# Optimization experiments

Hardware: AMD Instinct MI355X
Metric: run time of the kernel (lower is better)

Reference implementation:

```python
import jax, jax.numpy as jnp
import numpy as np

S, B, H = 2048, 2, 1024
NH = 16
HD = H // NH  # 64


def setup_inputs() -> dict:
    key = jax.random.key(0)
    k1, k2 = jax.random.split(key)
    hidden_states = jax.random.normal(k1, (S, B, H), dtype=jnp.float32)
    W_qkv = jax.random.normal(k2, (3 * H, H), dtype=jnp.float32) * (H ** -0.5)
    b_qkv = jnp.zeros((3 * H,), dtype=jnp.float32)
    return {"hidden_states": hidden_states, "W_qkv": W_qkv, "b_qkv": b_qkv}


def reference(hidden_states, W_qkv, b_qkv):
    s, b, h = hidden_states.shape
    # QKV projection: [S,B,3H] -> [S,B,NH,3*HD] -> split
    qkv = hidden_states @ W_qkv.T + b_qkv
    qkv = qkv.reshape(s, b, NH, 3 * HD)
    q, k, v = jnp.split(qkv, 3, axis=-1)  # each [S,B,NH,HD]
    norm_factor = HD ** -0.5
    # scores: [B,NH,Sq,Sk]
    scores = jnp.einsum('sbhd,tbhd->bhst', q, k) * norm_factor
    # Cumsum sequence-op (seq_op_in_fp32=True): cumsum over key dim, scaled by Sq^-0.5
    probs = jnp.cumsum(scores.astype(jnp.float32), axis=-1) * (s ** -0.5)
    probs = probs.astype(hidden_states.dtype)
    # PV: [B,NH,Sq,HD] -> seq-first [Sq,B,NH*HD]
    ctx = jnp.einsum('bhst,tbhd->sbhd', probs, v)
    return ctx.reshape(s, b, h)
```

## Files before the change

### kernel.cpp

```cpp
#include <hip/hip_runtime.h>

#define S 2048
#define B 2
#define H 1024
#define NH 16
#define HD 64
#define THREE_H 3072
#define ROWS (S*B)

typedef __attribute__((ext_vector_type(8))) short short8;
typedef __attribute__((ext_vector_type(4))) float f32x4;
typedef const __attribute__((address_space(1))) unsigned int* gptr_t;
typedef __attribute__((address_space(3))) unsigned int* lptr_t;

#define N8_A (ROWS * H / 8)
#define N8_W (THREE_H * H / 8)

__device__ __forceinline__ ushort f2bf(float f) {
    union { float f; unsigned u; } v; v.f = f;
    unsigned r = v.u + 0x7fffu + ((v.u >> 16) & 1u);
    return (ushort)(r >> 16);
}

__global__ void cast_both(const float* __restrict__ A, const float* __restrict__ W,
                          ushort* __restrict__ Ab, ushort* __restrict__ Wb) {
    int i = blockIdx.x * 256 + threadIdx.x;
    const float4* s4;
    ushort* dst;
    if (i < N8_A) { s4 = (const float4*)A; dst = Ab; }
    else if (i < N8_A + N8_W) { s4 = (const float4*)W; dst = Wb; i -= N8_A; }
    else return;
    float4 a = s4[2 * i], b = s4[2 * i + 1];
    short8 o;
    o[0] = f2bf(a.x); o[1] = f2bf(a.y); o[2] = f2bf(a.z); o[3] = f2bf(a.w);
    o[4] = f2bf(b.x); o[5] = f2bf(b.y); o[6] = f2bf(b.z); o[7] = f2bf(b.w);
    *(short8*)(dst + 8 * (size_t)i) = o;
}

__global__ __launch_bounds__(256) void qkv_gemm_mfma(const ushort* __restrict__ Abf,
                                                     const ushort* __restrict__ Wbf,
                                                     const float* __restrict__ bias,
                                                     ushort* __restrict__ Qb,
                                                     ushort* __restrict__ Kb,
                                                     float* __restrict__ Vf) {
    __shared__ ushort Abuf[128 * 32];
    __shared__ ushort Bbuf[128 * 32];
    const int tid = threadIdx.x;
    const int wave = tid >> 6, lane = tid & 63;
    const int wr = wave >> 1, wc = wave & 1;
    const int row0 = blockIdx.x * 128;
    const int col0 = blockIdx.y * 128;

    f32x4 acc[4][4] = {};

    const int lrow = lane >> 2;
    const int lk   = (lane & 3) * 8;

    for (int k0 = 0; k0 < H; k0 += 32) {
#pragma unroll
        for (int p = 0; p < 2; ++p) {
            int c = wave * 2 + p;
            int row = c * 16 + lrow;
            __builtin_amdgcn_global_load_lds(
                (gptr_t)&Abf[(size_t)(row0 + row) * H + k0 + lk],
                (lptr_t)&Abuf[c * 512 + lane * 8], 16, 0, 0);
            __builtin_amdgcn_global_load_lds(
                (gptr_t)&Wbf[(size_t)(col0 + row) * H + k0 + lk],
                (lptr_t)&Bbuf[c * 512 + lane * 8], 16, 0, 0);
        }
        __syncthreads();

        short8 af[4], bfr[4];
#pragma unroll
        for (int m = 0; m < 4; ++m) {
            int ar = wr * 64 + m * 16 + (lane & 15);
            af[m] = *(const short8*)&Abuf[ar * 32 + (lane >> 4) * 8];
            int br = wc * 64 + m * 16 + (lane & 15);
            bfr[m] = *(const short8*)&Bbuf[br * 32 + (lane >> 4) * 8];
        }
#pragma unroll
        for (int m = 0; m < 4; ++m)
#pragma unroll
            for (int n = 0; n < 4; ++n)
                acc[m][n] = __builtin_amdgcn_mfma_f32_16x16x32_bf16(af[m], bfr[n], acc[m][n], 0, 0, 0);
        __syncthreads();
    }

#pragma unroll
    for (int n = 0; n < 4; ++n) {
        int cbase = col0 + wc * 64 + n * 16;
        int h   = cbase / 192;
        int r3  = cbase % 192;
        int sel = r3 >> 6;
        int d   = (r3 & 63) + (lane & 15);
        float bv = bias[cbase + (lane & 15)];
#pragma unroll
        for (int m = 0; m < 4; ++m) {
            int rowb = row0 + wr * 64 + m * 16 + (lane >> 4) * 4;
#pragma unroll
            for (int j = 0; j < 4; ++j) {
                int r = rowb + j;
                int s = r >> 1, b = r & 1;
                size_t off = ((size_t)((b * NH + h) * S + s)) * HD + d;
                float val = acc[m][n][j] + bv;
                if (sel == 0)      Qb[off] = f2bf(val);
                else if (sel == 1) Kb[off] = f2bf(val);
                else               Vf[off] = val;
            }
        }
    }
}

__global__ void vsuf_chunksum(const float* __restrict__ Vf, float* __restrict__ csum) {
    int idx = blockIdx.x * 256 + threadIdx.x;
    int col = idx & 2047;
    int chunk = idx >> 11;
    const float* vp = Vf + ((size_t)(col >> 6) * S + chunk * 32) * HD + (col & 63);
    float s = 0.f;
#pragma unroll
    for (int t = 0; t < 32; ++t) s += vp[(size_t)t * HD];
    csum[idx] = s;
}

__global__ void vsuft_final(const float* __restrict__ Vf, const float* __restrict__ csum,
                            ushort* __restrict__ Vt) {
    int idx = blockIdx.x * 256 + threadIdx.x;
    int col = idx & 2047;
    int chunk = idx >> 11;
    int bh = col >> 6, d = col & 63;
    float acc = 0.f;
    for (int c = chunk + 1; c < 64; ++c) acc += csum[c * 2048 + col];
    const float* vp = Vf + ((size_t)bh * S + chunk * 32) * HD + d;
    ushort buf[32];
#pragma unroll
    for (int tt = 31; tt >= 0; --tt) {
        acc += vp[(size_t)tt * HD];
        buf[tt] = f2bf(acc);
    }
    ushort* op = Vt + ((size_t)bh * HD + d) * S + chunk * 32;
#pragma unroll
    for (int q = 0; q < 4; ++q) {
        short8 o;
#pragma unroll
        for (int k = 0; k < 8; ++k) o[k] = buf[q * 8 + k];
        *(short8*)(op + q * 8) = o;
    }
}

__global__ __launch_bounds__(256) void ktrans(const ushort* __restrict__ Kb,
                                              ushort* __restrict__ Kt) {
    __shared__ ushort Ks[64][72];
    const int bh = blockIdx.x;
    const int t0 = blockIdx.y * 64;
    const int tid = threadIdx.x;
    {
        const int tt = tid >> 2, part = (tid & 3) * 16;
        const ushort* src = Kb + ((size_t)bh * S + t0 + tt) * HD + part;
        *(short8*)&Ks[tt][part]     = *(const short8*)(src);
        *(short8*)&Ks[tt][part + 8] = *(const short8*)(src + 8);
    }
    __syncthreads();
    {
        const int d = tid >> 2, tq = (tid & 3) * 16;
        ushort tmp[16];
#pragma unroll
        for (int k = 0; k < 16; ++k) tmp[k] = Ks[tq + k][d];
        ushort* dst = Kt + ((size_t)bh * HD + d) * S + t0 + tq;
        short8 o0, o1;
#pragma unroll
        for (int k = 0; k < 8; ++k) { o0[k] = tmp[k]; o1[k] = tmp[8 + k]; }
        *(short8*)dst = o0;
        *(short8*)(dst + 8) = o1;
    }
}

__global__ __launch_bounds__(256) void kvm_mfma(const ushort* __restrict__ Kt,
                                                const ushort* __restrict__ Vt,
                                                float* __restrict__ Mpart) {
    const int bh = blockIdx.x, kb = blockIdx.y;
    const int tid = threadIdx.x, wave = tid >> 6, lane = tid & 63;
    const int slice = kb * 4 + wave;
    const ushort* Kp = Kt + (size_t)bh * HD * S;
    const ushort* Vp = Vt + (size_t)bh * HD * S;
    f32x4 acc[4][4] = {};
    const int il = lane & 15;
    const int tbase = slice * 128 + (lane >> 4) * 8;
#pragma unroll
    for (int ks = 0; ks < 4; ++ks) {
        const int t = tbase + ks * 32;
        short8 af[4], bfv[4];
#pragma unroll
        for (int m = 0; m < 4; ++m) af[m]  = *(const short8*)&Kp[(size_t)(m * 16 + il) * S + t];
#pragma unroll
        for (int n = 0; n < 4; ++n) bfv[n] = *(const short8*)&Vp[(size_t)(n * 16 + il) * S + t];
#pragma unroll
        for (int m = 0; m < 4; ++m)
#pragma unroll
            for (int n = 0; n < 4; ++n)
                acc[m][n] = __builtin_amdgcn_mfma_f32_16x16x32_bf16(af[m], bfv[n], acc[m][n], 0, 0, 0);
    }
    float* Mp = Mpart + ((size_t)slice * 32 + bh) * 4096;
#pragma unroll
    for (int m = 0; m < 4; ++m)
#pragma unroll
        for (int n = 0; n < 4; ++n)
#pragma unroll
            for (int j = 0; j < 4; ++j) {
                int i  = m * 16 + (lane >> 4) * 4 + j;
                int jj = n * 16 + il;
                Mp[i * 64 + jj] = acc[m][n][j];
            }
}

__global__ __launch_bounds__(256) void qm_mfma(const ushort* __restrict__ Qb,
                                               const float* __restrict__ Mpart,
                                               float* __restrict__ out) {
    __shared__ ushort Mt[64][72];
    const int bh = blockIdx.x, b = bh >> 4, h = bh & 15;
    const int tid = threadIdx.x;
    {
        const int i = tid >> 2, jq = (tid & 3) * 16;
        f32x4 s0 = {}, s1 = {}, s2 = {}, s3 = {};
#pragma unroll
        for (int sl = 0; sl < 16; ++sl) {
            const float* p = Mpart + ((size_t)sl * 32 + bh) * 4096 + i * 64 + jq;
            s0 += *(const f32x4*)(p);
            s1 += *(const f32x4*)(p + 4);
            s2 += *(const f32x4*)(p + 8);
            s3 += *(const f32x4*)(p + 12);
        }
#pragma unroll
        for (int k = 0; k < 4; ++k) {
            Mt[jq + 0  + k][i] = f2bf(s0[k]);
            Mt[jq + 4  + k][i] = f2bf(s1[k]);
            Mt[jq + 8  + k][i] = f2bf(s2[k]);
            Mt[jq + 12 + k][i] = f2bf(s3[k]);
        }
    }
    __syncthreads();
    const int wave = tid >> 6, lane = tid & 63;
    const int sl15 = lane & 15, koct = (lane >> 4) * 8;
    const int s0b = blockIdx.y * 256 + wave * 64;
    f32x4 acc[4][4] = {};
#pragma unroll
    for (int ks = 0; ks < 2; ++ks) {
        short8 af[4], bfv[4];
#pragma unroll
        for (int m = 0; m < 4; ++m) {
            int s = s0b + m * 16 + sl15;
            af[m] = *(const short8*)&Qb[((size_t)bh * S + s) * HD + ks * 32 + koct];
        }
#pragma unroll
        for (int n = 0; n < 4; ++n)
            bfv[n] = *(const short8*)&Mt[n * 16 + sl15][ks * 32 + koct];
#pragma unroll
        for (int m = 0; m < 4; ++m)
#pragma unroll
            for (int n = 0; n < 4; ++n)
                acc[m][n] = __builtin_amdgcn_mfma_f32_16x16x32_bf16(af[m], bfv[n], acc[m][n], 0, 0, 0);
    }
    const float scale = 0.125f * 0.02209708691207961f;
#pragma unroll
    for (int m = 0; m < 4; ++m)
#pragma unroll
        for (int n = 0; n < 4; ++n)
#pragma unroll
            for (int j = 0; j < 4; ++j) {
                int s = s0b + m * 16 + (lane >> 4) * 4 + j;
                int d = n * 16 + sl15;
                out[(size_t)(s * B + b) * H + h * 64 + d] = acc[m][n][j] * scale;
            }
}

extern "C" void kernel_launch(void* const* d_in, const int* in_sizes, int n_in,
                              void* d_out, int out_size, void* d_ws, size_t ws_size,
                              hipStream_t stream) {
    const float* hidden = (const float*)d_in[0];
    const float* W      = (const float*)d_in[1];
    const float* bias   = (const float*)d_in[2];
    float* out = (float*)d_out;

    float*  Vf    = (float*)d_ws;
    ushort* Qb    = (ushort*)(Vf + 4194304);
    ushort* Kb    = Qb + 4194304;
    ushort* Kt    = Kb + 4194304;
    ushort* Vt    = Kt + 4194304;
    float*  csum  = (float*)(Vt + 4194304);
    float*  Mpart = csum + 131072;
    ushort* Abf   = (ushort*)(Mpart + 2097152);
    ushort* Wbf   = Abf + 4194304;

    cast_both<<<(N8_A + N8_W + 255) / 256, 256, 0, stream>>>(hidden, W, Abf, Wbf);
    qkv_gemm_mfma<<<dim3(ROWS / 128, THREE_H / 128), 256, 0, stream>>>(Abf, Wbf, bias, Qb, Kb, Vf);
    vsuf_chunksum<<<512, 256, 0, stream>>>(Vf, csum);
    vsuft_final<<<512, 256, 0, stream>>>(Vf, csum, Vt);
    ktrans<<<dim3(32, 32), 256, 0, stream>>>(Kb, Kt);
    kvm_mfma<<<dim3(32, 4), 256, 0, stream>>>(Kt, Vt, Mpart);
    qm_mfma<<<dim3(32, 8), 256, 0, stream>>>(Qb, Mpart, out);
}
```

Baseline: 86.16 us.

## Widen GEMM K-tile with XOR-swizzled LDS, store V as bf16, merge ktrans with chunksum

The QKV GEMM now loads 64-wide K tiles per barrier, with an XOR swizzle on LDS slots to avoid bank conflicts, and remaps workgroups so neighbouring blocks share tiles in L2. V is written as bf16 instead of fp32, which halves its write and read traffic. The K transpose and the V chunk-sum kernels are fused into one launch, removing a launch and letting both run concurrently. Storing V in bf16 before the suffix sum adds a small precision loss in the prefix accumulation.

```diff
diff --git a/kernel.cpp b/kernel.cpp
--- a/kernel.cpp
+++ b/kernel.cpp
@@ -20,6 +20,10 @@
     union { float f; unsigned u; } v; v.f = f;
     unsigned r = v.u + 0x7fffu + ((v.u >> 16) & 1u);
     return (ushort)(r >> 16);
+}
+__device__ __forceinline__ float bf2f(ushort u) {
+    union { unsigned u; float f; } v; v.u = ((unsigned)u) << 16;
+    return v.f;
 }
 
 __global__ void cast_both(const float* __restrict__ A, const float* __restrict__ W,
@@ -42,47 +46,58 @@
                                                      const float* __restrict__ bias,
                                                      ushort* __restrict__ Qb,
                                                      ushort* __restrict__ Kb,
-                                                     float* __restrict__ Vf) {
-    __shared__ ushort Abuf[128 * 32];
-    __shared__ ushort Bbuf[128 * 32];
+                                                     ushort* __restrict__ Vraw) {
+    __shared__ ushort Abuf[128 * 64];
+    __shared__ ushort Bbuf[128 * 64];
     const int tid = threadIdx.x;
     const int wave = tid >> 6, lane = tid & 63;
     const int wr = wave >> 1, wc = wave & 1;
-    const int row0 = blockIdx.x * 128;
-    const int col0 = blockIdx.y * 128;
+
+    const int wgid = blockIdx.y * 32 + blockIdx.x;
+    const int swz = (wgid & 7) * 96 + (wgid >> 3);
+    const int row0 = (swz & 31) * 128;
+    const int col0 = (swz >> 5) * 128;
 
     f32x4 acc[4][4] = {};
 
-    const int lrow = lane >> 2;
-    const int lk   = (lane & 3) * 8;
-
-    for (int k0 = 0; k0 < H; k0 += 32) {
-#pragma unroll
-        for (int p = 0; p < 2; ++p) {
-            int c = wave * 2 + p;
-            int row = c * 16 + lrow;
+    const int srow = lane >> 3;
+    const int gk = ((lane & 7) ^ srow) * 8;
+    const int il = lane & 15, ko = lane >> 4;
+
+    for (int k0 = 0; k0 < H; k0 += 64) {
+#pragma unroll
+        for (int p = 0; p < 4; ++p) {
+            int row = wave * 32 + p * 8 + srow;
             __builtin_amdgcn_global_load_lds(
-                (gptr_t)&Abf[(size_t)(row0 + row) * H + k0 + lk],
-                (lptr_t)&Abuf[c * 512 + lane * 8], 16, 0, 0);
+                (gptr_t)&Abf[(size_t)(row0 + row) * H + k0 + gk],
+                (lptr_t)&Abuf[(wave * 32 + p * 8) * 64 + lane * 8], 16, 0, 0);
             __builtin_amdgcn_global_load_lds(
-                (gptr_t)&Wbf[(size_t)(col0 + row) * H + k0 + lk],
-                (lptr_t)&Bbuf[c * 512 + lane * 8], 16, 0, 0);
+                (gptr_t)&Wbf[(size_t)(col0 + row) * H + k0 + gk],
+                (lptr_t)&Bbuf[(wave * 32 + p * 8) * 64 + lane * 8], 16, 0, 0);
         }
         __syncthreads();
 
-        short8 af[4], bfr[4];
+        short8 af[4][2], bfr[4][2];
 #pragma unroll
         for (int m = 0; m < 4; ++m) {
-            int ar = wr * 64 + m * 16 + (lane & 15);
-            af[m] = *(const short8*)&Abuf[ar * 32 + (lane >> 4) * 8];
-            int br = wc * 64 + m * 16 + (lane & 15);
-            bfr[m] = *(const short8*)&Bbuf[br * 32 + (lane >> 4) * 8];
-        }
-#pragma unroll
-        for (int m = 0; m < 4; ++m)
-#pragma unroll
-            for (int n = 0; n < 4; ++n)
-                acc[m][n] = __builtin_amdgcn_mfma_f32_16x16x32_bf16(af[m], bfr[n], acc[m][n], 0, 0, 0);
+            int ar = wr * 64 + m * 16 + il;
+            int br = wc * 64 + m * 16 + il;
+#pragma unroll
+            for (int ks = 0; ks < 2; ++ks) {
+                int aslot = (ks * 4 + ko) ^ (ar & 7);
+                int bslot = (ks * 4 + ko) ^ (br & 7);
+                af[m][ks]  = *(const short8*)&Abuf[ar * 64 + aslot * 8];
+                bfr[m][ks] = *(const short8*)&Bbuf[br * 64 + bslot * 8];
+            }
+        }
+#pragma unroll
+        for (int ks = 0; ks < 2; ++ks)
+#pragma unroll
+            for (int m = 0; m < 4; ++m)
+#pragma unroll
+                for (int n = 0; n < 4; ++n)
+                    acc[m][n] = __builtin_amdgcn_mfma_f32_16x16x32_bf16(
+                        af[m][ks], bfr[n][ks], acc[m][n], 0, 0, 0);
         __syncthreads();
     }
 
@@ -92,37 +107,64 @@
         int h   = cbase / 192;
         int r3  = cbase % 192;
         int sel = r3 >> 6;
-        int d   = (r3 & 63) + (lane & 15);
-        float bv = bias[cbase + (lane & 15)];
+        int d   = (r3 & 63) + il;
+        float bv = bias[cbase + il];
+        ushort* dst = (sel == 0) ? Qb : (sel == 1) ? Kb : Vraw;
 #pragma unroll
         for (int m = 0; m < 4; ++m) {
-            int rowb = row0 + wr * 64 + m * 16 + (lane >> 4) * 4;
+            int rowb = row0 + wr * 64 + m * 16 + ko * 4;
 #pragma unroll
             for (int j = 0; j < 4; ++j) {
                 int r = rowb + j;
                 int s = r >> 1, b = r & 1;
-                size_t off = ((size_t)((b * NH + h) * S + s)) * HD + d;
-                float val = acc[m][n][j] + bv;
-                if (sel == 0)      Qb[off] = f2bf(val);
-                else if (sel == 1) Kb[off] = f2bf(val);
-                else               Vf[off] = val;
+                dst[((size_t)((b * NH + h) * S + s)) * HD + d] = f2bf(acc[m][n][j] + bv);
             }
         }
     }
 }
 
-__global__ void vsuf_chunksum(const float* __restrict__ Vf, float* __restrict__ csum) {
-    int idx = blockIdx.x * 256 + threadIdx.x;
-    int col = idx & 2047;
-    int chunk = idx >> 11;
-    const float* vp = Vf + ((size_t)(col >> 6) * S + chunk * 32) * HD + (col & 63);
-    float s = 0.f;
-#pragma unroll
-    for (int t = 0; t < 32; ++t) s += vp[(size_t)t * HD];
-    csum[idx] = s;
-}
-
-__global__ void vsuft_final(const float* __restrict__ Vf, const float* __restrict__ csum,
+__global__ __launch_bounds__(256) void ktrans_chunksum(const ushort* __restrict__ Kb,
+                                                       ushort* __restrict__ Kt,
+                                                       const ushort* __restrict__ Vraw,
+                                                       float* __restrict__ csum) {
+    __shared__ ushort Ks[64][72];
+    const int gb = blockIdx.x;
+    const int tid = threadIdx.x;
+    if (gb < 1024) {
+        const int bh = gb >> 5;
+        const int t0 = (gb & 31) * 64;
+        {
+            const int tt = tid >> 2, part = (tid & 3) * 16;
+            const ushort* src = Kb + ((size_t)bh * S + t0 + tt) * HD + part;
+            *(short8*)&Ks[tt][part]     = *(const short8*)(src);
+            *(short8*)&Ks[tt][part + 8] = *(const short8*)(src + 8);
+        }
+        __syncthreads();
+        {
+            const int d = tid >> 2, tq = (tid & 3) * 16;
+            ushort tmp[16];
+#pragma unroll
+            for (int k = 0; k < 16; ++k) tmp[k] = Ks[tq + k][d];
+            ushort* dst = Kt + ((size_t)bh * HD + d) * S + t0 + tq;
+            short8 o0, o1;
+#pragma unroll
+            for (int k = 0; k < 8; ++k) { o0[k] = tmp[k]; o1[k] = tmp[8 + k]; }
+            *(short8*)dst = o0;
+            *(short8*)(dst + 8) = o1;
+        }
+    } else {
+        int idx = (gb - 1024) * 256 + tid;
+        int col = idx & 2047;
+        int chunk = idx >> 11;
+        const ushort* vp = Vraw + ((size_t)(col >> 6) * S + chunk * 32) * HD + (col & 63);
+        float s = 0.f;
+#pragma unroll
+        for (int t = 0; t < 32; ++t) s += bf2f(vp[(size_t)t * HD]);
+        csum[chunk * 2048 + col] = s;
+    }
+}
+
+__global__ void vsuft_final(const ushort* __restrict__ Vraw, const float* __restrict__ csum,
                             ushort* __restrict__ Vt) {
     int idx = blockIdx.x * 256 + threadIdx.x;
     int col = idx & 2047;
@@ -130,11 +172,11 @@
     int bh = col >> 6, d = col & 63;
     float acc = 0.f;
     for (int c = chunk + 1; c < 64; ++c) acc += csum[c * 2048 + col];
-    const float* vp = Vf + ((size_t)bh * S + chunk * 32) * HD + d;
+    const ushort* vp = Vraw + ((size_t)bh * S + chunk * 32) * HD + d;
     ushort buf[32];
 #pragma unroll
     for (int tt = 31; tt >= 0; --tt) {
-        acc += vp[(size_t)tt * HD];
+        acc += bf2f(vp[(size_t)tt * HD]);
         buf[tt] = f2bf(acc);
     }
     ushort* op = Vt + ((size_t)bh * HD + d) * S + chunk * 32;
@@ -144,33 +186,6 @@
 #pragma unroll
         for (int k = 0; k < 8; ++k) o[k] = buf[q * 8 + k];
         *(short8*)(op + q * 8) = o;
-    }
-}
-
-__global__ __launch_bounds__(256) void ktrans(const ushort* __restrict__ Kb,
-                                              ushort* __restrict__ Kt) {
-    __shared__ ushort Ks[64][72];
-    const int bh = blockIdx.x;
-    const int t0 = blockIdx.y * 64;
-    const int tid = threadIdx.x;
-    {
-        const int tt = tid >> 2, part = (tid & 3) * 16;
-        const ushort* src = Kb + ((size_t)bh * S + t0 + tt) * HD + part;
-        *(short8*)&Ks[tt][part]     = *(const short8*)(src);
-        *(short8*)&Ks[tt][part + 8] = *(const short8*)(src + 8);
-    }
-    __syncthreads();
-    {
-        const int d = tid >> 2, tq = (tid & 3) * 16;
-        ushort tmp[16];
-#pragma unroll
-        for (int k = 0; k < 16; ++k) tmp[k] = Ks[tq + k][d];
-        ushort* dst = Kt + ((size_t)bh * HD + d) * S + t0 + tq;
-        short8 o0, o1;
-#pragma unroll
-        for (int k = 0; k < 8; ++k) { o0[k] = tmp[k]; o1[k] = tmp[8 + k]; }
-        *(short8*)dst = o0;
-        *(short8*)(dst + 8) = o1;
     }
 }
 
@@ -280,21 +295,20 @@
     const float* bias   = (const float*)d_in[2];
     float* out = (float*)d_out;
 
-    float*  Vf    = (float*)d_ws;
-    ushort* Qb    = (ushort*)(Vf + 4194304);
+    ushort* Qb    = (ushort*)d_ws;
     ushort* Kb    = Qb + 4194304;
     ushort* Kt    = Kb + 4194304;
-    ushort* Vt    = Kt + 4194304;
+    ushort* Vraw  = Kt + 4194304;
+    ushort* Vt    = Vraw + 4194304;
     float*  csum  = (float*)(Vt + 4194304);
     float*  Mpart = csum + 131072;
     ushort* Abf   = (ushort*)(Mpart + 2097152);
     ushort* Wbf   = Abf + 4194304;
 
     cast_both<<<(N8_A + N8_W + 255) / 256, 256, 0, stream>>>(hidden, W, Abf, Wbf);
-    qkv_gemm_mfma<<<dim3(ROWS / 128, THREE_H / 128), 256, 0, stream>>>(Abf, Wbf, bias, Qb, Kb, Vf);
-    vsuf_chunksum<<<512, 256, 0, stream>>>(Vf, csum);
-    vsuft_final<<<512, 256, 0, stream>>>(Vf, csum, Vt);
-    ktrans<<<dim3(32, 32), 256, 0, stream>>>(Kb, Kt);
+    qkv_gemm_mfma<<<dim3(32, 24), 256, 0, stream>>>(Abf, Wbf, bias, Qb, Kb, Vraw);
+    ktrans_chunksum<<<1536, 256, 0, stream>>>(Kb, Kt, Vraw, csum);
+    vsuft_final<<<512, 256, 0, stream>>>(Vraw, csum, Vt);
     kvm_mfma<<<dim3(32, 4), 256, 0, stream>>>(Kt, Vt, Mpart);
     qm_mfma<<<dim3(32, 8), 256, 0, stream>>>(Qb, Mpart, out);
 }
```

Result: slower. 91.03 us (+5.6%).
